# Kernel optimization log

Hardware: AMD Instinct MI355X
Metric: run time of the kernel (lower is better)

The kernel has to match this reference:

```python
import jax, jax.numpy as jnp
import numpy as np

B, S, H, M, E = 8, 2048, 2048, 256, 8
Hh = H // 2

def setup_inputs() -> dict:
    key = jax.random.key(0)
    ks = jax.random.split(key, 12)
    s = 0.02
    return {
        "x":   jax.random.normal(ks[0], (B, S, H), dtype=jnp.float32),
        # metacognitive (router) network: H -> M -> M -> E, softmax
        "Wm1": jax.random.normal(ks[1], (H, M), dtype=jnp.float32) * s,
        "bm1": jnp.zeros((M,), dtype=jnp.float32),
        "Wm2": jax.random.normal(ks[2], (M, M), dtype=jnp.float32) * s,
        "bm2": jnp.zeros((M,), dtype=jnp.float32),
        "Wm3": jax.random.normal(ks[3], (M, E), dtype=jnp.float32) * s,
        "bm3": jnp.zeros((E,), dtype=jnp.float32),
        # stacked expert MLPs: Linear(H,H/2)-ReLU-Linear(H/2,H)-Tanh
        "W1":  jax.random.normal(ks[4], (E, H, Hh), dtype=jnp.float32) * s,
        "b1":  jnp.zeros((E, Hh), dtype=jnp.float32),
        "W2":  jax.random.normal(ks[5], (E, Hh, H), dtype=jnp.float32) * s,
        "b2":  jnp.zeros((E, H), dtype=jnp.float32),
        # strategy_effectiveness buffer (init: ones)
        "eff": jnp.ones((E,), dtype=jnp.float32),
    }

def reference(x, Wm1, bm1, Wm2, bm2, Wm3, bm3, W1, b1, W2, b2, eff):
    # --- select_strategy ---
    pooled = x.mean(axis=1)                                   # [B,H]
    h = jax.nn.relu(pooled @ Wm1 + bm1)                       # [B,M]
    h = jax.nn.relu(h @ Wm2 + bm2)                            # [B,M]
    probs = jax.nn.softmax(h @ Wm3 + bm3, axis=-1)            # [B,E]
    w = jax.nn.softmax(probs * eff[None, :], axis=-1)         # [B,E]
    # --- apply_strategies (all experts batched) ---
    he = jax.nn.relu(jnp.einsum('bsh,ehf->bsef', x, W1) + b1) # [B,S,E,Hh]
    ye = jnp.tanh(jnp.einsum('bsef,efh->bseh', he, W2) + b2)  # [B,S,E,H]
    out = jnp.einsum('bseh,be->bsh', ye, w)                   # [B,S,H]
    return out
```

## Files before the change

### kernel.cpp

```cpp
#include <hip/hip_runtime.h>
#include <hip/hip_bf16.h>
#include <cstdint>
#include <cstddef>

#define B_   8
#define S_   2048
#define H_   2048
#define M_   256
#define E_   8
#define HH_  1024
#define BS_  (B_*S_)

typedef _Float16 f16;
typedef _Float16 f16x8 __attribute__((ext_vector_type(8)));
typedef _Float16 f16x4 __attribute__((ext_vector_type(4)));
typedef float    f32x4 __attribute__((ext_vector_type(4)));

#define HSLOT 32768

__device__ __forceinline__ void gl_lds16(const void* g, void* l) {
  __builtin_amdgcn_global_load_lds(
      (const __attribute__((address_space(1))) uint32_t*)g,
      (__attribute__((address_space(3))) uint32_t*)l, 16, 0, 0);
}

__device__ __forceinline__ float fast_tanh(float x) {
  float t = __expf(2.f * x);
  float r = __builtin_amdgcn_rcpf(t + 1.f);
  return __builtin_fmaf(-2.f, r, 1.f);
}

template<int NG, bool SEG, int KB, class F>
__device__ __forceinline__ void kloop(const char* aBlk, const char* bBlk,
                                      char* ldsc, f32x4 (&acc)[8][4], F&& fold) {
  constexpr int NH = NG * 2;
  const int tid = threadIdx.x, ln = tid & 63, wv = tid >> 6;
  const int l15 = ln & 15, kq = ln >> 4;
  const int wm = wv >> 2, wn = wv & 3;

  const char* aPc[2]; const char* bPc[2];
#pragma unroll
  for (int j = 0; j < 2; ++j) {
    int row = (tid >> 2) + j * 128;
    int kqs = (tid & 3) ^ ((row >> 1) & 3);
    aPc[j] = aBlk + (size_t)row * KB + kqs * 16;
    bPc[j] = bBlk + (size_t)row * KB + kqs * 16;
  }
  const int rowA = wm * 128 + l15;
  const int rowB = wn * 64 + l15;
  const int aRd = rowA * 64 + ((kq ^ ((rowA >> 1) & 3)) << 4);
  const int bRd = 16384 + rowB * 64 + ((kq ^ ((rowB >> 1) & 3)) << 4);
  const int dst0 = tid * 16;

  auto stage2 = [&](int Ht, int op) {
    if (Ht >= NH) return;
    char* sb = ldsc + (Ht & 3) * HSLOT;
    size_t oa, ob;
    if constexpr (SEG) {
      size_t kb = (size_t)((Ht & 31) * 64);
      oa = ((size_t)(Ht >> 5) << 25) + kb;
      ob = ((size_t)(Ht >> 5) << 22) + kb;
    } else { oa = ob = (size_t)Ht * 64; }
    if (op == 0) {
      gl_lds16(aPc[0] + oa, sb + dst0);
      gl_lds16(aPc[1] + oa, sb + 8192 + dst0);
    } else {
      gl_lds16(bPc[0] + ob, sb + 16384 + dst0);
      gl_lds16(bPc[1] + ob, sb + 24576 + dst0);
    }
  };

#pragma unroll
  for (int Ht = 0; Ht < 3; ++Ht) { stage2(Ht, 0); stage2(Ht, 1); }
  asm volatile("s_waitcnt vmcnt(8)" ::: "memory");
  __builtin_amdgcn_s_barrier();

#pragma unroll 1
  for (int g = 0; g < NG; ++g) {
#pragma unroll
    for (int kh = 0; kh < 2; ++kh) {
      const int H = g * 2 + kh;
      const char* sb = ldsc + (H & 3) * HSLOT;
      f16x8 bf[4];
#pragma unroll
      for (int mh = 0; mh < 2; ++mh) {
        f16x8 af[4];
        const char* ab = sb + aRd + mh * 4096;
#pragma unroll
        for (int m = 0; m < 4; ++m) af[m] = *(const f16x8*)(ab + m * 1024);
        if (mh == 0) {
          const char* bb = sb + bRd;
#pragma unroll
          for (int n = 0; n < 4; ++n) bf[n] = *(const f16x8*)(bb + n * 1024);
        }
        stage2(H + 3, mh);
        __builtin_amdgcn_s_barrier();
        asm volatile("s_waitcnt lgkmcnt(0)" ::: "memory");
        __builtin_amdgcn_sched_barrier(0);
        __builtin_amdgcn_s_setprio(1);
#pragma unroll
        for (int m = 0; m < 4; ++m)
#pragma unroll
          for (int n = 0; n < 4; ++n)
            acc[mh * 4 + m][n] = __builtin_amdgcn_mfma_f32_16x16x32_f16(
                af[m], bf[n], acc[mh * 4 + m][n], 0, 0, 0);
        __builtin_amdgcn_s_setprio(0);
        __builtin_amdgcn_sched_barrier(0);
        if (mh == 1) {
          if (H < NH - 3)       { asm volatile("s_waitcnt vmcnt(8)" ::: "memory"); }
          else if (H == NH - 3) { asm volatile("s_waitcnt vmcnt(4)" ::: "memory"); }
          else if (H == NH - 2) { asm volatile("s_waitcnt vmcnt(0)" ::: "memory"); }
        }
        __builtin_amdgcn_s_barrier();
      }
    }
    if constexpr (SEG) { if ((g & 15) == 15) fold(g >> 4); }
  }
}

__global__ __launch_bounds__(512, 2) void gemm1_t8(
    const f16* __restrict__ xf, const f16* __restrict__ W1t,
    const float* __restrict__ b1, f16* __restrict__ he) {
  __shared__ alignas(16) char ldsc[4 * HSLOT];
  int id = blockIdx.x;
  int logical = (id & 7) * 256 + (id >> 3);
  int e = logical >> 8, mt = (logical >> 2) & 63, nt = logical & 3;
  int brow = mt * 256, bcol = nt * 256;

  const char* aBlk = (const char*)xf + (size_t)brow * 4096;
  const char* bBlk = (const char*)W1t + ((size_t)e << 22) + (size_t)bcol * 4096;

  f32x4 acc[8][4] = {};
  kloop<32, false, 4096>(aBlk, bBlk, ldsc, acc, [](int) {});

  const int tid = threadIdx.x, ln = tid & 63, wv = tid >> 6;
  const int l15 = ln & 15, kq4 = (ln >> 4) * 4;
  const int wm = wv >> 2, wn = wv & 3;
  f16* C = he + ((size_t)e << 24);
#pragma unroll
  for (int n = 0; n < 4; ++n) {
    int gc = bcol + wn * 64 + n * 16 + l15;
    float bias = b1[e * HH_ + gc];
#pragma unroll
    for (int m = 0; m < 8; ++m) {
      int gr0 = brow + wm * 128 + m * 16 + kq4;
#pragma unroll
      for (int r = 0; r < 4; ++r)
        C[(size_t)(gr0 + r) * HH_ + gc] = (f16)fmaxf(acc[m][n][r] + bias, 0.f);
    }
  }
}

__global__ __launch_bounds__(512, 2) void gemm2_t8(
    const f16* __restrict__ he, const f16* __restrict__ W2t,
    const float* __restrict__ b2, const float* __restrict__ wbuf,
    float* __restrict__ out) {
  __shared__ alignas(16) char ldsc[4 * HSLOT];
  __shared__ float biasLDS[E_][256];
  __shared__ float wLDS[E_];
  int id = blockIdx.x;
  int logical = (id & 7) * 64 + (id >> 3);
  int mt = logical >> 3, nt = logical & 7;
  int brow = mt * 256, bcol = nt * 256;
  int bb = brow >> 11;

  const int tid = threadIdx.x, ln = tid & 63, wv = tid >> 6;
  const int l15 = ln & 15, kq4 = (ln >> 4) * 4;
  const int wm = wv >> 2, wn = wv & 3;

  {
    int i = tid;
#pragma unroll
    for (int rep = 0; rep < 4; ++rep, i += 512)
      biasLDS[i >> 8][i & 255] = b2[(size_t)(i >> 8) * H_ + bcol + (i & 255)];
    if (tid < E_) wLDS[tid] = wbuf[bb * E_ + tid];
  }
  __syncthreads();

  const char* aBlk = (const char*)he + (size_t)brow * 2048;
  const char* bBlk = (const char*)W2t + (size_t)bcol * 2048;

  f32x4 acc[8][4] = {};
  f16x4 tot[8][4] = {};

  auto fold = [&](int e) {
    float we = wLDS[e];
#pragma unroll
    for (int n = 0; n < 4; ++n) {
      float bias = biasLDS[e][wn * 64 + n * 16 + l15];
#pragma unroll
      for (int m = 0; m < 8; ++m) {
#pragma unroll
        for (int r = 0; r < 4; ++r) {
          tot[m][n][r] += (f16)(we * fast_tanh(acc[m][n][r] + bias));
          acc[m][n][r] = 0.f;
        }
      }
    }
  };

  kloop<128, true, 2048>(aBlk, bBlk, ldsc, acc, fold);

#pragma unroll
  for (int n = 0; n < 4; ++n) {
    int gc = bcol + wn * 64 + n * 16 + l15;
#pragma unroll
    for (int m = 0; m < 8; ++m) {
      int gr0 = brow + wm * 128 + m * 16 + kq4;
#pragma unroll
      for (int r = 0; r < 4; ++r)
        out[(size_t)(gr0 + r) * H_ + gc] = (float)tot[m][n][r];
    }
  }
}

__global__ void convert_x_pool(const float* __restrict__ x, f16* __restrict__ xf,
                               float* __restrict__ partial) {
  int h  = blockIdx.x * 256 + threadIdx.x;
  int sc = blockIdx.y;
  int b  = blockIdx.z;
  size_t base = ((size_t)b * S_ + sc * 64) * H_ + h;
  float sum = 0.f;
#pragma unroll 4
  for (int i = 0; i < 64; ++i) {
    float v = x[base + (size_t)i * H_];
    sum += v;
    xf[base + (size_t)i * H_] = (f16)v;
  }
  partial[((size_t)b * H_ + h) * 32 + sc] = sum;
}

__global__ void router_kernel(const float* __restrict__ partial,
                              const float* __restrict__ Wm1, const float* __restrict__ bm1,
                              const float* __restrict__ Wm2, const float* __restrict__ bm2,
                              const float* __restrict__ Wm3, const float* __restrict__ bm3,
                              const float* __restrict__ eff, float* __restrict__ wout) {
  __shared__ float pl[H_];
  __shared__ float h1[M_];
  __shared__ float h2[M_];
  __shared__ float lg[E_];
  int b = blockIdx.x;
  int t = threadIdx.x;

  for (int i = t; i < H_; i += 256) {
    float s = 0.f;
    const float* p = partial + ((size_t)b * H_ + i) * 32;
#pragma unroll
    for (int c = 0; c < 32; ++c) s += p[c];
    pl[i] = s * (1.0f / S_);
  }
  __syncthreads();

  float s = bm1[t];
  for (int k = 0; k < H_; ++k) s += pl[k] * Wm1[(size_t)k * M_ + t];
  h1[t] = fmaxf(s, 0.f);
  __syncthreads();

  s = bm2[t];
  for (int k = 0; k < M_; ++k) s += h1[k] * Wm2[k * M_ + t];
  h2[t] = fmaxf(s, 0.f);
  __syncthreads();

  if (t < E_) {
    float l = bm3[t];
    for (int k = 0; k < M_; ++k) l += h2[k] * Wm3[k * E_ + t];
    lg[t] = l;
  }
  __syncthreads();

  if (t == 0) {
    float p[E_], q[E_];
    float mx = -1e30f;
    for (int e = 0; e < E_; ++e) mx = fmaxf(mx, lg[e]);
    float den = 0.f;
    for (int e = 0; e < E_; ++e) { p[e] = __expf(lg[e] - mx); den += p[e]; }
    float inv = 1.f / den;
    for (int e = 0; e < E_; ++e) q[e] = p[e] * inv * eff[e];
    mx = -1e30f;
    for (int e = 0; e < E_; ++e) mx = fmaxf(mx, q[e]);
    den = 0.f;
    for (int e = 0; e < E_; ++e) { q[e] = __expf(q[e] - mx); den += q[e]; }
    inv = 1.f / den;
    for (int e = 0; e < E_; ++e) wout[b * E_ + e] = q[e] * inv;
  }
}

__global__ void transpose_cvt(const float* __restrict__ in, f16* __restrict__ out,
                              int R, int C) {
  __shared__ f16 tile[32][33];
  int e  = blockIdx.z;
  int c0 = blockIdx.x * 32, r0 = blockIdx.y * 32;
  int tx = threadIdx.x & 31, ty = threadIdx.x >> 5;
  const float* inp = in + (size_t)e * R * C;
  f16* outp = out + (size_t)e * R * C;
#pragma unroll
  for (int i = 0; i < 4; ++i) {
    int r = r0 + ty + i * 8;
    tile[ty + i * 8][tx] = (f16)inp[(size_t)r * C + c0 + tx];
  }
  __syncthreads();
#pragma unroll
  for (int i = 0; i < 4; ++i) {
    int c = c0 + ty + i * 8;
    outp[(size_t)c * R + r0 + tx] = tile[tx][ty + i * 8];
  }
}

extern "C" void kernel_launch(void* const* d_in, const int* in_sizes, int n_in,
                              void* d_out, int out_size, void* d_ws, size_t ws_size,
                              hipStream_t stream) {
  const float* x   = (const float*)d_in[0];
  const float* Wm1 = (const float*)d_in[1];
  const float* bm1 = (const float*)d_in[2];
  const float* Wm2 = (const float*)d_in[3];
  const float* bm2 = (const float*)d_in[4];
  const float* Wm3 = (const float*)d_in[5];
  const float* bm3 = (const float*)d_in[6];
  const float* W1  = (const float*)d_in[7];
  const float* b1  = (const float*)d_in[8];
  const float* W2  = (const float*)d_in[9];
  const float* b2  = (const float*)d_in[10];
  const float* eff = (const float*)d_in[11];
  float* out = (float*)d_out;

  char* ws = (char*)d_ws;
  size_t off = 0;
  auto take = [&](size_t bytes) { void* p = ws + off; off += (bytes + 255) & ~(size_t)255; return p; };

  f16*   xf      = (f16*)  take((size_t)BS_ * H_ * 2);
  f16*   W1t     = (f16*)  take((size_t)E_ * HH_ * H_ * 2);
  f16*   W2t     = (f16*)  take((size_t)E_ * H_ * HH_ * 2);
  float* partial = (float*)take((size_t)B_ * H_ * 32 * 4);
  float* wbuf    = (float*)take(1024);
  f16*   he      = (f16*)  take((size_t)E_ * BS_ * HH_ * 2);

  convert_x_pool<<<dim3(H_ / 256, S_ / 64, B_), 256, 0, stream>>>(x, xf, partial);
  router_kernel<<<B_, 256, 0, stream>>>(partial, Wm1, bm1, Wm2, bm2, Wm3, bm3, eff, wbuf);
  transpose_cvt<<<dim3(HH_ / 32, H_ / 32, E_), 256, 0, stream>>>(W1, W1t, H_, HH_);
  transpose_cvt<<<dim3(H_ / 32, HH_ / 32, E_), 256, 0, stream>>>(W2, W2t, HH_, H_);

  gemm1_t8<<<2048, 512, 0, stream>>>(xf, W1t, b1, he);
  gemm2_t8<<<512, 512, 0, stream>>>(he, W2t, b2, wbuf, out);
}
```

Baseline: 1.336 ms.

## Rewrite expert GEMM1 with 256x128 tiles, double-buffered LDS and higher occupancy

Replaces the first expert GEMM's 256x256 tile kernel with a 256x128 tile kernel that uses its own simple double-buffered LDS loop (48 KB) and a launch bound of 4 blocks per CU, doubling the grid to 4096 blocks. The goal is more occupancy to hide latency, in exchange for less operand reuse per tile and a full vmcnt(0) wait plus barrier every K step. Output stores in both GEMMs become nontemporal to avoid polluting cache with the large intermediate and output tensors.

```diff
diff --git a/kernel.cpp b/kernel.cpp
--- a/kernel.cpp
+++ b/kernel.cpp
@@ -17,6 +17,7 @@
 typedef float    f32x4 __attribute__((ext_vector_type(4)));
 
 #define HSLOT 32768
+#define HS2   24576
 
 __device__ __forceinline__ void gl_lds16(const void* g, void* l) {
   __builtin_amdgcn_global_load_lds(
@@ -118,35 +119,86 @@
   }
 }
 
-__global__ __launch_bounds__(512, 2) void gemm1_t8(
+__global__ __launch_bounds__(512, 4) void gemm1_v9(
     const f16* __restrict__ xf, const f16* __restrict__ W1t,
     const float* __restrict__ b1, f16* __restrict__ he) {
-  __shared__ alignas(16) char ldsc[4 * HSLOT];
+  __shared__ alignas(16) char ldsc[2 * HS2];
   int id = blockIdx.x;
-  int logical = (id & 7) * 256 + (id >> 3);
-  int e = logical >> 8, mt = (logical >> 2) & 63, nt = logical & 3;
-  int brow = mt * 256, bcol = nt * 256;
+  int logical = (id & 7) * 512 + (id >> 3);
+  int e = logical >> 9, mt = (logical >> 3) & 63, nt = logical & 7;
+  int brow = mt * 256, bcol = nt * 128;
+
+  const int tid = threadIdx.x, ln = tid & 63, wv = tid >> 6;
+  const int l15 = ln & 15, kq = ln >> 4;
+  const int wm = wv >> 1, wn = wv & 1;
 
   const char* aBlk = (const char*)xf + (size_t)brow * 4096;
   const char* bBlk = (const char*)W1t + ((size_t)e << 22) + (size_t)bcol * 4096;
 
-  f32x4 acc[8][4] = {};
-  kloop<32, false, 4096>(aBlk, bBlk, ldsc, acc, [](int) {});
-
-  const int tid = threadIdx.x, ln = tid & 63, wv = tid >> 6;
-  const int l15 = ln & 15, kq4 = (ln >> 4) * 4;
-  const int wm = wv >> 2, wn = wv & 3;
+  const char* aPc[2]; const char* bPc;
+#pragma unroll
+  for (int j = 0; j < 2; ++j) {
+    int row = (tid >> 2) + j * 128;
+    int kqs = (tid & 3) ^ ((row >> 1) & 3);
+    aPc[j] = aBlk + (size_t)row * 4096 + kqs * 16;
+  }
+  { int row = tid >> 2;
+    int kqs = (tid & 3) ^ ((row >> 1) & 3);
+    bPc = bBlk + (size_t)row * 4096 + kqs * 16; }
+
+  const int rowA = wm * 64 + l15;
+  const int rowB = wn * 64 + l15;
+  const int aRd = rowA * 64 + ((kq ^ ((rowA >> 1) & 3)) << 4);
+  const int bRd = 16384 + rowB * 64 + ((kq ^ ((rowB >> 1) & 3)) << 4);
+  const int dst0 = tid * 16;
+
+  auto stage = [&](int Ht) {
+    if (Ht >= 64) return;
+    char* sb = ldsc + (Ht & 1) * HS2;
+    size_t ko = (size_t)Ht * 64;
+    gl_lds16(aPc[0] + ko, sb + dst0);
+    gl_lds16(aPc[1] + ko, sb + 8192 + dst0);
+    gl_lds16(bPc + ko, sb + 16384 + dst0);
+  };
+
+  f32x4 acc[4][4] = {};
+  stage(0);
+  asm volatile("s_waitcnt vmcnt(0)" ::: "memory");
+  __builtin_amdgcn_s_barrier();
+
+#pragma unroll 1
+  for (int H = 0; H < 64; ++H) {
+    const char* sb = ldsc + (H & 1) * HS2;
+    f16x8 af[4], bf[4];
+#pragma unroll
+    for (int m = 0; m < 4; ++m) af[m] = *(const f16x8*)(sb + aRd + m * 1024);
+#pragma unroll
+    for (int n = 0; n < 4; ++n) bf[n] = *(const f16x8*)(sb + bRd + n * 1024);
+    stage(H + 1);
+    __builtin_amdgcn_s_setprio(1);
+#pragma unroll
+    for (int m = 0; m < 4; ++m)
+#pragma unroll
+      for (int n = 0; n < 4; ++n)
+        acc[m][n] = __builtin_amdgcn_mfma_f32_16x16x32_f16(af[m], bf[n], acc[m][n], 0, 0, 0);
+    __builtin_amdgcn_s_setprio(0);
+    asm volatile("s_waitcnt vmcnt(0)" ::: "memory");
+    __builtin_amdgcn_s_barrier();
+  }
+
+  const int kq4 = kq * 4;
   f16* C = he + ((size_t)e << 24);
 #pragma unroll
   for (int n = 0; n < 4; ++n) {
     int gc = bcol + wn * 64 + n * 16 + l15;
     float bias = b1[e * HH_ + gc];
 #pragma unroll
-    for (int m = 0; m < 8; ++m) {
-      int gr0 = brow + wm * 128 + m * 16 + kq4;
+    for (int m = 0; m < 4; ++m) {
+      int gr0 = brow + wm * 64 + m * 16 + kq4;
 #pragma unroll
       for (int r = 0; r < 4; ++r)
-        C[(size_t)(gr0 + r) * HH_ + gc] = (f16)fmaxf(acc[m][n][r] + bias, 0.f);
+        __builtin_nontemporal_store((f16)fmaxf(acc[m][n][r] + bias, 0.f),
+                                    &C[(size_t)(gr0 + r) * HH_ + gc]);
     }
   }
 }
@@ -209,7 +261,8 @@
       int gr0 = brow + wm * 128 + m * 16 + kq4;
 #pragma unroll
       for (int r = 0; r < 4; ++r)
-        out[(size_t)(gr0 + r) * H_ + gc] = (float)tot[m][n][r];
+        __builtin_nontemporal_store((float)tot[m][n][r],
+                                    &out[(size_t)(gr0 + r) * H_ + gc]);
     }
   }
 }
@@ -339,6 +392,6 @@
   transpose_cvt<<<dim3(HH_ / 32, H_ / 32, E_), 256, 0, stream>>>(W1, W1t, H_, HH_);
   transpose_cvt<<<dim3(H_ / 32, HH_ / 32, E_), 256, 0, stream>>>(W2, W2t, HH_, H_);
 
-  gemm1_t8<<<2048, 512, 0, stream>>>(xf, W1t, b1, he);
+  gemm1_v9<<<4096, 512, 0, stream>>>(xf, W1t, b1, he);
   gemm2_t8<<<512, 512, 0, stream>>>(he, W2t, b2, wbuf, out);
 }
```

Result: slower. 1.455 ms (+8.9%).
